# Optimization experiments

Hardware: AMD Instinct MI355X
Metric: run time of the kernel (lower is better)

The kernel has to match this reference:

```python
import jax, jax.numpy as jnp
import numpy as np


def setup_inputs() -> dict:
    key = jax.random.key(0)
    B, C, H, W = 16, 512, 56, 56
    heads, agent, win = 8, 49, 56
    ks = jax.random.split(key, 16)
    std = 0.02
    tn = lambda k, s: jax.random.truncated_normal(k, -2.0, 2.0, s, jnp.float32) * std
    return {
        "x": jax.random.normal(ks[0], (B, C, H, W), jnp.float32),
        "H": H,
        "W": W,
        "q_w": jax.random.normal(ks[1], (C, C), jnp.float32) * (C ** -0.5),
        "kv_w": jax.random.normal(ks[2], (2 * C, C), jnp.float32) * (C ** -0.5),
        "proj_w": jax.random.normal(ks[3], (C, C), jnp.float32) * (C ** -0.5),
        "proj_b": jnp.zeros((C,), jnp.float32),
        "dwc_w": jax.random.normal(ks[4], (C, 1, 3, 3), jnp.float32) * (1.0 / 3.0),
        "dwc_b": jnp.zeros((C,), jnp.float32),
        "an_bias": tn(ks[5], (heads, agent, 7, 7)),
        "na_bias": tn(ks[6], (heads, agent, 7, 7)),
        "ah_bias": tn(ks[7], (1, heads, agent, win, 1)),
        "aw_bias": tn(ks[8], (1, heads, agent, 1, win)),
        "ha_bias": tn(ks[9], (1, heads, win, 1, agent)),
        "wa_bias": tn(ks[10], (1, heads, 1, win, agent)),
    }


def reference(x, H, W, q_w, kv_w, proj_w, proj_b, dwc_w, dwc_b,
              an_bias, na_bias, ah_bias, aw_bias, ha_bias, wa_bias):
    B, C, H1, W1 = x.shape
    heads, agent = an_bias.shape[0], an_bias.shape[1]
    hd = C // heads
    scale = hd ** -0.5
    n = H1 * W1
    pool = int(agent ** 0.5)  # 7

    # NOTE: original torch code does x.view(B, H1*W1, C) on an NCHW tensor:
    # a raw row-major reshape, reproduced faithfully here.
    xf = x.reshape(B, n, C)

    q = xf @ q_w.T                       # [B, n, C]
    kv = xf @ kv_w.T                     # [B, n, 2C]
    k, v = kv[..., :C], kv[..., C:]

    # agent tokens: adaptive avg pool of q (as HxW image) to pool x pool (exact blocks)
    q_img = q.reshape(B, H, W, C)
    agent_tokens = q_img.reshape(B, pool, H // pool, pool, W // pool, C).mean(axis=(2, 4))
    agent_tokens = agent_tokens.reshape(B, agent, C)

    qh = q.reshape(B, n, heads, hd).transpose(0, 2, 1, 3)            # [B,h,n,d]
    kh = k.reshape(B, n, heads, hd).transpose(0, 2, 1, 3)            # [B,h,n,d]
    vh = v.reshape(B, n, heads, hd).transpose(0, 2, 1, 3)            # [B,h,n,d]
    ah = agent_tokens.reshape(B, agent, heads, hd).transpose(0, 2, 1, 3)  # [B,h,a,d]

    # stage 1: agent -> kv attention, with interpolated + separable position bias
    pb1 = jax.image.resize(an_bias, (heads, agent, H, W), 'bilinear').reshape(1, heads, agent, n)
    pb2 = (ah_bias + aw_bias).reshape(1, heads, agent, n)
    agent_logits = jnp.einsum('bhad,bhnd->bhan', ah * scale, kh) + pb1 + pb2
    agent_attn = jax.nn.softmax(agent_logits, axis=-1)
    agent_v = jnp.einsum('bhan,bhnd->bhad', agent_attn, vh)          # [B,h,a,d]

    # stage 2: query -> agent attention
    ab1 = jax.image.resize(na_bias, (heads, agent, H, W), 'bilinear').reshape(1, heads, agent, n)
    ab1 = ab1.transpose(0, 1, 3, 2)                                  # [1,h,n,a]
    ab2 = (ha_bias + wa_bias).reshape(1, heads, n, agent)
    q_logits = jnp.einsum('bhnd,bhad->bhna', qh * scale, ah) + ab1 + ab2
    q_attn = jax.nn.softmax(q_logits, axis=-1)
    out = jnp.einsum('bhna,bhad->bhnd', q_attn, agent_v)
    out = out.transpose(0, 2, 1, 3).reshape(B, n, C)

    # depthwise-conv residual on v (sr_ratio == 1: no interpolate)
    v_img = v.reshape(B, H, W, C).transpose(0, 3, 1, 2)              # [B,C,H,W]
    dwc = jax.lax.conv_general_dilated(
        v_img, dwc_w, window_strides=(1, 1), padding='SAME',
        feature_group_count=C, dimension_numbers=('NCHW', 'OIHW', 'NCHW'))
    dwc = dwc + dwc_b[None, :, None, None]
    out = out + dwc.transpose(0, 2, 3, 1).reshape(B, n, C)

    out = out @ proj_w.T + proj_b
    return out.reshape(B, C, H1, W1)
```

## Files before the change

### kernel.cpp

```cpp
#include <hip/hip_runtime.h>
#include <math.h>

#define B_ 16
#define C_ 512
#define Nn 3136
#define HEADS 8
#define HD 64
#define AG 49
#define Mrows (B_ * Nn)

typedef unsigned short ushortT;
typedef __attribute__((ext_vector_type(8))) short bf16x8;
typedef __attribute__((ext_vector_type(4))) float f32x4;

#define MFMA16(a, b, c) __builtin_amdgcn_mfma_f32_16x16x32_bf16((a), (b), (c), 0, 0, 0)

__device__ inline float bf2f(ushortT u) { return __uint_as_float(((unsigned)u) << 16); }
__device__ inline ushortT f2bf(float f) {
    unsigned x = __float_as_uint(f);
    unsigned r = (x + 0x7fffu + ((x >> 16) & 1u)) >> 16;
    return (ushortT)r;
}
__device__ inline f32x4 fzero4() { f32x4 z = {0.f, 0.f, 0.f, 0.f}; return z; }

__device__ inline void gl_lds16(const ushortT* g, ushortT* l) {
    __builtin_amdgcn_global_load_lds(
        (const __attribute__((address_space(1))) void*)g,
        (__attribute__((address_space(3))) void*)l, 16, 0, 0);
}

#define VMCNT(n) asm volatile("s_waitcnt vmcnt(" #n ")" ::: "memory")
#define LGKM0_SB() { asm volatile("s_waitcnt lgkmcnt(0)" ::: "memory"); \
                     __builtin_amdgcn_sched_barrier(0); }
#define BAR() __builtin_amdgcn_s_barrier()

__global__ void cvt_f2b4(const float* __restrict__ src, ushortT* __restrict__ dst, int n4) {
    int g = blockIdx.x * 256 + threadIdx.x;
    if (g >= n4) return;
    float4 v = *(const float4*)&src[(size_t)g * 4];
    ushort4 o = make_ushort4(f2bf(v.x), f2bf(v.y), f2bf(v.z), f2bf(v.w));
    *(ushort4*)&dst[(size_t)g * 4] = o;
}

__global__ void repack_w(const float* __restrict__ w, float* __restrict__ wT) {
    int g = blockIdx.x * 256 + threadIdx.x;
    if (g >= 9 * 512) return;
    int c = g % 512, tap = g / 512;
    wT[g] = w[c * 9 + tap];
}

template <int MB, int NL>
__device__ __forceinline__ void quad(f32x4 (&acc)[8][4], const bf16x8 (&af)[4][2],
                                     const bf16x8 (&bf)[4][2]) {
#pragma unroll
    for (int m = 0; m < 4; ++m)
#pragma unroll
        for (int n = 0; n < 2; ++n) {
            acc[MB + m][NL + n] = MFMA16(af[m][0], bf[NL + n][0], acc[MB + m][NL + n]);
            acc[MB + m][NL + n] = MFMA16(af[m][1], bf[NL + n][1], acc[MB + m][NL + n]);
        }
}

template <typename TO>
__global__ __launch_bounds__(512, 2)
void gemm256(const ushortT* __restrict__ A, const ushortT* __restrict__ Bw,
             const float* __restrict__ bias, TO* __restrict__ out,
             int N, int nbn) {
    __shared__ __align__(16) ushortT As[2][16384];
    __shared__ __align__(16) ushortT Bs[2][16384];
    const int t = threadIdx.x, lane = t & 63, wid = t >> 6;
    const int chunk = (int)gridDim.x >> 3;
    const int id2 = ((int)blockIdx.x & 7) * chunk + ((int)blockIdx.x >> 3);
    const int by = id2 / nbn, bx = id2 - by * nbn;
    const int m0 = by * 256, n0 = bx * 256;
    const int wm = wid >> 2, wn = wid & 3;

    const int rl0 = t >> 3;
    const int skg = (t & 7) ^ (rl0 & 7);
    const int ra0 = rl0 & 63;
    const int ra1 = (rl0 & 63) + 128;
    const int rb0 = (rl0 & 31) + ((rl0 >> 5) << 6);
    const int rb1 = rb0 + 128;
    const ushortT* gA0 = A + (size_t)(m0 + ra0) * 512 + skg * 8;
    const ushortT* gA1 = A + (size_t)(m0 + ra1) * 512 + skg * 8;
    const ushortT* gB0 = Bw + (size_t)(n0 + rb0) * 512 + skg * 8;
    const ushortT* gB1 = Bw + (size_t)(n0 + rb1) * 512 + skg * 8;
    const int bA0 = wid * 512;
    const int bA1 = wid * 512 + 8192;
    const int gbu = ((wid * 8) & 31) + (((wid * 8) >> 5) << 6);
    const int bB0 = gbu * 64;
    const int bB1 = bB0 + 8192;

#define ISSA(bufi, ro, ko) { gl_lds16(gA0 + (ro) * 512 + (ko), &As[bufi][bA0 + (ro) * 64]); \
                             gl_lds16(gA1 + (ro) * 512 + (ko), &As[bufi][bA1 + (ro) * 64]); }
#define ISSB(bufi, ro, ko) { gl_lds16(gB0 + (ro) * 512 + (ko), &Bs[bufi][bB0 + (ro) * 64]); \
                             gl_lds16(gB1 + (ro) * 512 + (ko), &Bs[bufi][bB1 + (ro) * 64]); }

    f32x4 acc[8][4];
#pragma unroll
    for (int i = 0; i < 8; ++i)
#pragma unroll
        for (int j = 0; j < 4; ++j) acc[i][j] = fzero4();

    const int r15 = lane & 15, kq16 = lane >> 4;
    const int rA = wm * 128 + r15;
    const int rB = wn * 64 + r15;
    const int sw0 = ((kq16) ^ (r15 & 7)) << 3;
    const int sw1 = ((4 + kq16) ^ (r15 & 7)) << 3;

    ISSA(0, 0, 0);
    ISSB(0, 0, 0);
    ISSB(0, 32, 0);
    ISSA(0, 64, 0);
    VMCNT(4);
    BAR();

    bf16x8 af[4][2], bf[4][2];
    for (int kt = 0; kt < 8; ++kt) {
        const ushortT* Ac = As[kt & 1];
        const ushortT* Bc = Bs[kt & 1];
        const int nb = (kt + 1) & 1;
        const int ko = (kt + 1) * 64;
        const bool pre = (kt < 7);
#pragma unroll
        for (int mt = 0; mt < 4; ++mt) {
            af[mt][0] = *(const bf16x8*)&Ac[(rA + mt * 16) * 64 + sw0];
            af[mt][1] = *(const bf16x8*)&Ac[(rA + mt * 16) * 64 + sw1];
        }
#pragma unroll
        for (int nt = 0; nt < 2; ++nt) {
            bf[nt][0] = *(const bf16x8*)&Bc[(rB + nt * 16) * 64 + sw0];
            bf[nt][1] = *(const bf16x8*)&Bc[(rB + nt * 16) * 64 + sw1];
        }
        if (pre) ISSA(nb, 0, ko);
        BAR(); LGKM0_SB();
        __builtin_amdgcn_s_setprio(1);
        quad<0, 0>(acc, af, bf);
        __builtin_amdgcn_s_setprio(0);
        if (pre) { VMCNT(4); } else { VMCNT(2); }
        BAR();
#pragma unroll
        for (int nt = 2; nt < 4; ++nt) {
            bf[nt][0] = *(const bf16x8*)&Bc[(rB + nt * 16) * 64 + sw0];
            bf[nt][1] = *(const bf16x8*)&Bc[(rB + nt * 16) * 64 + sw1];
        }
        if (pre) ISSB(nb, 0, ko);
        BAR(); LGKM0_SB();
        __builtin_amdgcn_s_setprio(1);
        quad<0, 2>(acc, af, bf);
        __builtin_amdgcn_s_setprio(0);
        if (pre) { VMCNT(4); } else { VMCNT(0); }
        BAR();
#pragma unroll
        for (int mt = 0; mt < 4; ++mt) {
            af[mt][0] = *(const bf16x8*)&Ac[(rA + 64 + mt * 16) * 64 + sw0];
            af[mt][1] = *(const bf16x8*)&Ac[(rA + 64 + mt * 16) * 64 + sw1];
        }
        if (pre) ISSB(nb, 32, ko);
        BAR(); LGKM0_SB();
        __builtin_amdgcn_s_setprio(1);
        quad<4, 0>(acc, af, bf);
        __builtin_amdgcn_s_setprio(0);
        BAR();
        if (pre) ISSA(nb, 64, ko);
        BAR(); LGKM0_SB();
        __builtin_amdgcn_s_setprio(1);
        quad<4, 2>(acc, af, bf);
        __builtin_amdgcn_s_setprio(0);
        if (pre) { VMCNT(4); }
        BAR();
    }
#undef ISSA
#undef ISSB

    const int cn = r15, rg = kq16 << 2;
#pragma unroll
    for (int mt = 0; mt < 8; ++mt) {
        int mrow = m0 + wm * 128 + mt * 16 + rg;
#pragma unroll
        for (int nt = 0; nt < 4; ++nt) {
            int ncol = n0 + wn * 64 + nt * 16 + cn;
            float bv = bias ? bias[ncol] : 0.f;
#pragma unroll
            for (int r = 0; r < 4; ++r) {
                float v = acc[mt][nt][r] + bv;
                if (sizeof(TO) == 2) ((ushortT*)out)[(size_t)(mrow + r) * N + ncol] = f2bf(v);
                else                 ((float*)out)[(size_t)(mrow + r) * N + ncol] = v;
            }
        }
    }
}

__global__ void agent_pool(const ushortT* __restrict__ qkv, float* __restrict__ at) {
    int g = blockIdx.x * 256 + threadIdx.x;
    int c8 = (g & 63) << 3;
    int a = (g >> 6) % AG;
    int b = g / (AG * 64);
    int p1 = a / 7, p2 = a % 7;
    float s[8] = {};
    for (int yy = 0; yy < 8; ++yy)
#pragma unroll
        for (int xx = 0; xx < 8; ++xx) {
            int i = (p1 * 8 + yy) * 56 + (p2 * 8 + xx);
            const ushortT* p = &qkv[(size_t)(b * Nn + i) * 1536 + c8];
            ushort4 u0 = *(const ushort4*)p;
            ushort4 u1 = *(const ushort4*)(p + 4);
            s[0] += bf2f(u0.x); s[1] += bf2f(u0.y); s[2] += bf2f(u0.z); s[3] += bf2f(u0.w);
            s[4] += bf2f(u1.x); s[5] += bf2f(u1.y); s[6] += bf2f(u1.z); s[7] += bf2f(u1.w);
        }
    float* o = &at[((size_t)(b * AG + a) << 9) + c8];
#pragma unroll
    for (int j = 0; j < 8; ++j) o[j] = s[j] * (1.f / 64.f);
}

__device__ inline float bilin7(const float* __restrict__ p, int y, int x) {
    float fy = fminf(fmaxf(y * 0.125f - 0.4375f, 0.f), 6.f);
    float fx = fminf(fmaxf(x * 0.125f - 0.4375f, 0.f), 6.f);
    int y0 = (int)fy; float ty = fy - y0; int y1 = min(y0 + 1, 6);
    int x0 = (int)fx; float tx = fx - x0; int x1 = min(x0 + 1, 6);
    float v00 = p[y0 * 7 + x0], v01 = p[y0 * 7 + x1];
    float v10 = p[y1 * 7 + x0], v11 = p[y1 * 7 + x1];
    return (1.f - ty) * ((1.f - tx) * v00 + tx * v01) + ty * ((1.f - tx) * v10 + tx * v11);
}

__global__ void bias1_k(const float* __restrict__ an, const float* __restrict__ ahb,
                        const float* __restrict__ awb, float* __restrict__ out) {
    int g = blockIdx.x * 256 + threadIdx.x;
    if (g >= HEADS * AG * Nn) return;
    int i = g % Nn; int a = (g / Nn) % AG; int h = g / (AG * Nn);
    int y = i / 56, x = i % 56;
    float v = bilin7(an + (h * AG + a) * 49, y, x);
    out[g] = v + ahb[(h * AG + a) * 56 + y] + awb[(h * AG + a) * 56 + x];
}

__global__ void bias2_k(const float* __restrict__ na, const float* __restrict__ hab,
                        const float* __restrict__ wab, float* __restrict__ out) {
    int g = blockIdx.x * 256 + threadIdx.x;
    if (g >= HEADS * Nn * AG) return;
    int a = g % AG; int i = (g / AG) % Nn; int h = g / (AG * Nn);
    int y = i / 56, x = i % 56;
    float v = bilin7(na + (h * AG + a) * 49, y, x);
    out[g] = v + hab[(h * 56 + y) * AG + a] + wab[(h * 56 + x) * AG + a];
}

__global__ void zerof(float* __restrict__ p, int nfl) {
    int g = blockIdx.x * 256 + threadIdx.x;
    if (g < nfl) p[g] = 0.f;
}

__global__ __launch_bounds__(256)
void agent_av_fused(const ushortT* __restrict__ qkv, const float* __restrict__ at,
                    const float* __restrict__ b1, float* __restrict__ num,
                    float* __restrict__ den) {
    __shared__ __align__(16) ushortT ah_s[64 * 72];
    __shared__ __align__(16) ushortT vt[64 * 72];
    __shared__ __align__(16) ushortT p_s[64 * 72];
    const int t = threadIdx.x, lane = t & 63, wid = t >> 6;
    const int bh = blockIdx.y, b = bh >> 3, h = bh & 7;
    for (int idx = t; idx < 512; idx += 256) {
        int a = idx >> 3, d8 = (idx & 7) << 3;
        bf16x8 tmp;
        if (a < AG) {
            const float* p = &at[((size_t)(b * AG + a) << 9) + (h << 6) + d8];
#pragma unroll
            for (int j = 0; j < 8; ++j) tmp[j] = (short)f2bf(p[j] * 0.125f);
        } else {
#pragma unroll
            for (int j = 0; j < 8; ++j) tmp[j] = 0;
        }
        *(bf16x8*)&ah_s[a * 72 + d8] = tmp;
    }
    __syncthreads();
    const int r15 = lane & 15, kq = (lane >> 4) << 3;
    const int rbase = (lane >> 4) << 2;
    bf16x8 af[4][2];
#pragma unroll
    for (int mt = 0; mt < 4; ++mt)
#pragma unroll
        for (int ks = 0; ks < 2; ++ks)
            af[mt][ks] = *(const bf16x8*)&ah_s[(mt * 16 + r15) * 72 + ks * 32 + kq];

    f32x4 accn[4];
#pragma unroll
    for (int nt = 0; nt < 4; ++nt) accn[nt] = fzero4();
    float denl[4][4];
#pragma unroll
    for (int mt = 0; mt < 4; ++mt)
#pragma unroll
        for (int r = 0; r < 4; ++r) denl[mt][r] = 0.f;

    const int i0b = blockIdx.x * 448;
    const int svi = t >> 2, svd = (t & 3) << 4;
    for (int cc = 0; cc < 7; ++cc) {
        const int i0 = i0b + cc * 64;
        {
            const ushortT* vp = &qkv[(size_t)(b * Nn + i0 + svi) * 1536 + 1024 + (h << 6) + svd];
            bf16x8 u0 = *(const bf16x8*)vp;
            bf16x8 u1 = *(const bf16x8*)(vp + 8);
#pragma unroll
            for (int j = 0; j < 8; ++j) {
                vt[(svd + j) * 72 + svi]     = (ushortT)u0[j];
                vt[(svd + 8 + j) * 72 + svi] = (ushortT)u1[j];
            }
        }
        {
            const int iw = i0 + wid * 16;
            const ushortT* kp = &qkv[(size_t)(b * Nn + iw + r15) * 1536 + 512 + (h << 6) + kq];
            bf16x8 bk0 = *(const bf16x8*)kp;
            bf16x8 bk1 = *(const bf16x8*)(kp + 32);
            f32x4 sacc[4];
#pragma unroll
            for (int mt = 0; mt < 4; ++mt) {
                sacc[mt] = MFMA16(af[mt][0], bk0, fzero4());
                sacc[mt] = MFMA16(af[mt][1], bk1, sacc[mt]);
            }
            const int ic = iw + r15;
#pragma unroll
            for (int mt = 0; mt < 4; ++mt)
#pragma unroll
                for (int r = 0; r < 4; ++r) {
                    int a = mt * 16 + rbase + r;
                    float e = 0.f;
                    if (a < AG)
                        e = __expf(sacc[mt][r] + b1[(size_t)(h * AG + a) * Nn + ic]);
                    denl[mt][r] += e;
                    p_s[a * 72 + wid * 16 + r15] = f2bf(e);
                }
        }
        __syncthreads();
        {
            bf16x8 ap0 = *(const bf16x8*)&p_s[(wid * 16 + r15) * 72 + kq];
            bf16x8 ap1 = *(const bf16x8*)&p_s[(wid * 16 + r15) * 72 + 32 + kq];
#pragma unroll
            for (int nt = 0; nt < 4; ++nt) {
                bf16x8 bv0 = *(const bf16x8*)&vt[(nt * 16 + r15) * 72 + kq];
                bf16x8 bv1 = *(const bf16x8*)&vt[(nt * 16 + r15) * 72 + 32 + kq];
                accn[nt] = MFMA16(ap0, bv0, accn[nt]);
                accn[nt] = MFMA16(ap1, bv1, accn[nt]);
            }
        }
        __syncthreads();
    }
#pragma unroll
    for (int r = 0; r < 4; ++r) {
        int a = wid * 16 + rbase + r;
        if (a < AG) {
#pragma unroll
            for (int nt = 0; nt < 4; ++nt)
                atomicAdd(&num[((size_t)(bh * AG + a) << 6) + nt * 16 + r15],
                          accn[nt][r]);
        }
    }
#pragma unroll
    for (int mt = 0; mt < 4; ++mt)
#pragma unroll
        for (int r = 0; r < 4; ++r) {
            float s = denl[mt][r];
#pragma unroll
            for (int off = 8; off >= 1; off >>= 1) s += __shfl_xor(s, off);
            if (r15 == 0) {
                int a = mt * 16 + rbase + r;
                if (a < AG) atomicAdd(&den[bh * AG + a], s);
            }
        }
}

__global__ __launch_bounds__(256)
void q_attn_mfma(const ushortT* __restrict__ qkv, const float* __restrict__ at,
                 const float* __restrict__ num, const float* __restrict__ den,
                 const float* __restrict__ b2, ushortT* __restrict__ attn) {
    __shared__ __align__(16) ushortT ah_s[64 * 72];
    __shared__ __align__(16) ushortT avT[64 * 72];
    __shared__ __align__(16) ushortT p_s[4][16 * 72];
    int t = threadIdx.x, lane = t & 63, wid = t >> 6;
    int bh = blockIdx.y, b = bh >> 3, h = bh & 7;
    for (int idx = t; idx < 512; idx += 256) {
        int a = idx >> 3, d8 = (idx & 7) << 3;
        bf16x8 tmp;
        if (a < AG) {
            const float* p = &at[((size_t)(b * AG + a) << 9) + (h << 6) + d8];
#pragma unroll
            for (int j = 0; j < 8; ++j) tmp[j] = (short)f2bf(p[j] * 0.125f);
        } else {
#pragma unroll
            for (int j = 0; j < 8; ++j) tmp[j] = 0;
        }
        *(bf16x8*)&ah_s[a * 72 + d8] = tmp;
    }
    for (int idx = t; idx < 4096; idx += 256) {
        int a = idx >> 6, d = idx & 63;
        float v = 0.f;
        if (a < AG)
            v = num[((size_t)(bh * AG + a) << 6) + d] / den[bh * AG + a];
        avT[d * 72 + a] = f2bf(v);
    }
    __syncthreads();
    int r15 = lane & 15, kq = (lane >> 4) << 3;
    bf16x8 bah[4][2], bav[4][2];
#pragma unroll
    for (int nt = 0; nt < 4; ++nt)
#pragma unroll
        for (int ks = 0; ks < 2; ++ks) {
            bah[nt][ks] = *(const bf16x8*)&ah_s[(nt * 16 + r15) * 72 + ks * 32 + kq];
            bav[nt][ks] = *(const bf16x8*)&avT[(nt * 16 + r15) * 72 + ks * 32 + kq];
        }
    ushortT* psw = p_s[wid];
    int i0b = blockIdx.x * 448;
    int rbase = (lane >> 4) << 2;
    for (int tt = 0; tt < 7; ++tt) {
        int i0 = i0b + (wid * 7 + tt) * 16;
        const ushortT* qp = &qkv[(size_t)(b * Nn + i0 + r15) * 1536 + (h << 6) + kq];
        bf16x8 aq0 = *(const bf16x8*)qp;
        bf16x8 aq1 = *(const bf16x8*)(qp + 32);
        f32x4 lg[4];
#pragma unroll
        for (int nt = 0; nt < 4; ++nt) {
            lg[nt] = MFMA16(aq0, bah[nt][0], fzero4());
            lg[nt] = MFMA16(aq1, bah[nt][1], lg[nt]);
        }
        float p4[4][4];
#pragma unroll
        for (int r = 0; r < 4; ++r) {
            int i = i0 + rbase + r;
            float vals[4]; float sm = 0.f;
#pragma unroll
            for (int nt = 0; nt < 4; ++nt) {
                int a = nt * 16 + r15;
                float e = 0.f;
                if (a < AG) e = __expf(lg[nt][r] + b2[(size_t)(h * Nn + i) * AG + a]);
                vals[nt] = e; sm += e;
            }
#pragma unroll
            for (int off = 8; off >= 1; off >>= 1) sm += __shfl_xor(sm, off);
            float inv = 1.f / sm;
#pragma unroll
            for (int nt = 0; nt < 4; ++nt) p4[nt][r] = vals[nt] * inv;
        }
#pragma unroll
        for (int nt = 0; nt < 4; ++nt)
#pragma unroll
            for (int r = 0; r < 4; ++r)
                psw[(rbase + r) * 72 + nt * 16 + r15] = f2bf(p4[nt][r]);
        bf16x8 ap0 = *(const bf16x8*)&psw[r15 * 72 + kq];
        bf16x8 ap1 = *(const bf16x8*)&psw[r15 * 72 + 32 + kq];
        f32x4 ov[4];
#pragma unroll
        for (int nt = 0; nt < 4; ++nt) {
            ov[nt] = MFMA16(ap0, bav[nt][0], fzero4());
            ov[nt] = MFMA16(ap1, bav[nt][1], ov[nt]);
        }
#pragma unroll
        for (int r = 0; r < 4; ++r) {
            int i = i0 + rbase + r;
            ushortT* op = &attn[(size_t)(b * Nn + i) * C_ + (h << 6)];
#pragma unroll
            for (int nt = 0; nt < 4; ++nt)
                op[nt * 16 + r15] = f2bf(ov[nt][r]);
        }
    }
}

__global__ void dwc_add_v(const ushortT* __restrict__ qkv, const float* __restrict__ wT,
                          const float* __restrict__ bb, ushortT* __restrict__ attn) {
    int g = blockIdx.x * 256 + threadIdx.x;
    int c8 = (g & 63) << 3;
    int bi = g >> 6;
    int i = bi % Nn;
    int y = i / 56, x = i % 56;
    float acc[8];
    {
        float4 b0 = *(const float4*)&bb[c8];
        float4 b1 = *(const float4*)&bb[c8 + 4];
        acc[0] = b0.x; acc[1] = b0.y; acc[2] = b0.z; acc[3] = b0.w;
        acc[4] = b1.x; acc[5] = b1.y; acc[6] = b1.z; acc[7] = b1.w;
    }
#pragma unroll
    for (int dy = -1; dy <= 1; ++dy) {
        int yy = y + dy; if (yy < 0 || yy > 55) continue;
#pragma unroll
        for (int dx = -1; dx <= 1; ++dx) {
            int xx = x + dx; if (xx < 0 || xx > 55) continue;
            const ushortT* vp = &qkv[(size_t)(bi + dy * 56 + dx) * 1536 + 1024 + c8];
            ushort4 u0 = *(const ushort4*)vp;
            ushort4 u1 = *(const ushort4*)(vp + 4);
            const float* wp = &wT[((dy + 1) * 3 + dx + 1) * 512 + c8];
            float4 w0 = *(const float4*)wp;
            float4 w1 = *(const float4*)(wp + 4);
            acc[0] += bf2f(u0.x) * w0.x; acc[1] += bf2f(u0.y) * w0.y;
            acc[2] += bf2f(u0.z) * w0.z; acc[3] += bf2f(u0.w) * w0.w;
            acc[4] += bf2f(u1.x) * w1.x; acc[5] += bf2f(u1.y) * w1.y;
            acc[6] += bf2f(u1.z) * w1.z; acc[7] += bf2f(u1.w) * w1.w;
        }
    }
    ushortT* op = &attn[(size_t)bi * C_ + c8];
    ushort4 a0 = *(const ushort4*)op;
    ushort4 a1 = *(const ushort4*)(op + 4);
    ushort4 o0 = make_ushort4(f2bf(bf2f(a0.x) + acc[0]), f2bf(bf2f(a0.y) + acc[1]),
                              f2bf(bf2f(a0.z) + acc[2]), f2bf(bf2f(a0.w) + acc[3]));
    ushort4 o1 = make_ushort4(f2bf(bf2f(a1.x) + acc[4]), f2bf(bf2f(a1.y) + acc[5]),
                              f2bf(bf2f(a1.z) + acc[6]), f2bf(bf2f(a1.w) + acc[7]));
    *(ushort4*)op = o0; *(ushort4*)(op + 4) = o1;
}

extern "C" void kernel_launch(void* const* d_in, const int* in_sizes, int n_in,
                              void* d_out, int out_size, void* d_ws, size_t ws_size,
                              hipStream_t stream) {
    const float* x      = (const float*)d_in[0];
    const float* q_w    = (const float*)d_in[3];
    const float* kv_w   = (const float*)d_in[4];
    const float* proj_w = (const float*)d_in[5];
    const float* proj_b = (const float*)d_in[6];
    const float* dwc_w  = (const float*)d_in[7];
    const float* dwc_b  = (const float*)d_in[8];
    const float* an_b   = (const float*)d_in[9];
    const float* na_b   = (const float*)d_in[10];
    const float* ah_b   = (const float*)d_in[11];
    const float* aw_b   = (const float*)d_in[12];
    const float* ha_b   = (const float*)d_in[13];
    const float* wa_b   = (const float*)d_in[14];
    float* out = (float*)d_out;

    char* ws = (char*)d_ws;
    ushortT* R    = (ushortT*)(ws);
    ushortT* qkv  = (ushortT*)(ws + 51380224);
    ushortT* Wqkv = (ushortT*)(ws + 205520896);
    ushortT* Wp   = (ushortT*)(ws + 207093760);
    float*   wT   = (float*)(ws + 207618048);
    float*   at   = (float*)(ws + 207636480);
    float*   b1   = (float*)(ws + 209242112);
    float*   b2   = (float*)(ws + 214159360);
    float*   num  = (float*)(ws + 219076608);
    float*   den  = (float*)Wqkv;
    ushortT* xb   = R;
    ushortT* attn = R;

    cvt_f2b4<<<25088, 256, 0, stream>>>(x, xb, 6422528);
    cvt_f2b4<<<256,   256, 0, stream>>>(q_w, Wqkv, 65536);
    cvt_f2b4<<<512,   256, 0, stream>>>(kv_w, Wqkv + 262144, 131072);
    cvt_f2b4<<<256,   256, 0, stream>>>(proj_w, Wp, 65536);
    repack_w<<<18,    256, 0, stream>>>(dwc_w, wT);
    gemm256<ushortT><<<1176, 512, 0, stream>>>(xb, Wqkv, nullptr, qkv, 1536, 6);
    agent_pool<<<196, 256, 0, stream>>>(qkv, at);
    bias1_k<<<4802, 256, 0, stream>>>(an_b, ah_b, aw_b, b1);
    bias2_k<<<4802, 256, 0, stream>>>(na_b, ha_b, wa_b, b2);
    zerof<<<1568, 256, 0, stream>>>(num, B_ * HEADS * AG * HD);
    zerof<<<25,   256, 0, stream>>>(den, B_ * HEADS * AG);
    agent_av_fused<<<dim3(7, 128), 256, 0, stream>>>(qkv, at, b1, num, den);
    q_attn_mfma<<<dim3(7, 128), 256, 0, stream>>>(qkv, at, num, den, b2, attn);
    dwc_add_v<<<12544, 256, 0, stream>>>(qkv, wT, dwc_b, attn);
    gemm256<float><<<392, 512, 0, stream>>>(attn, Wp, proj_b, out, 512, 2);
}
```

Before: 536.9 us.

## Merge small kernels, parallelize agent pooling, and simplify GEMM prefetch schedule

Weight conversions, the two bias-map kernels and the two zero-fill kernels are each folded into a single launch to cut launch overhead. The agent pooling kernel now gives each (batch, agent) pair its own block, splitting the 64 pooled positions across four thread groups and combining them with a shared-memory reduction, so far more blocks run in parallel. The QKV/proj GEMM main loop issues the whole next tile's A and B loads early and waits once per iteration instead of interleaving waits. This may expose more memory latency or reduce overlap at the single wait point.

```diff
diff --git a/kernel.cpp b/kernel.cpp
--- a/kernel.cpp
+++ b/kernel.cpp
@@ -42,11 +42,24 @@
     *(ushort4*)&dst[(size_t)g * 4] = o;
 }
 
-__global__ void repack_w(const float* __restrict__ w, float* __restrict__ wT) {
+__global__ void cvt_weights(const float* __restrict__ qw, const float* __restrict__ kvw,
+                            const float* __restrict__ pw, const float* __restrict__ dwcw,
+                            ushortT* __restrict__ Wqkv, ushortT* __restrict__ Wp,
+                            float* __restrict__ wT) {
     int g = blockIdx.x * 256 + threadIdx.x;
-    if (g >= 9 * 512) return;
-    int c = g % 512, tap = g / 512;
-    wT[g] = w[c * 9 + tap];
+    if (g < 196608) {
+        const float* src = (g < 65536) ? &qw[(size_t)g * 4] : &kvw[(size_t)(g - 65536) * 4];
+        float4 v = *(const float4*)src;
+        *(ushort4*)&Wqkv[(size_t)g * 4] =
+            make_ushort4(f2bf(v.x), f2bf(v.y), f2bf(v.z), f2bf(v.w));
+    } else if (g < 262144) {
+        float4 v = *(const float4*)&pw[(size_t)(g - 196608) * 4];
+        *(ushort4*)&Wp[(size_t)(g - 196608) * 4] =
+            make_ushort4(f2bf(v.x), f2bf(v.y), f2bf(v.z), f2bf(v.w));
+    } else {
+        int gg = g - 262144;
+        if (gg < 4608) { int c = gg & 511, tap = gg >> 9; wT[gg] = dwcw[c * 9 + tap]; }
+    }
 }
 
 template <int MB, int NL>
@@ -108,11 +121,9 @@
     const int sw0 = ((kq16) ^ (r15 & 7)) << 3;
     const int sw1 = ((4 + kq16) ^ (r15 & 7)) << 3;
 
-    ISSA(0, 0, 0);
-    ISSB(0, 0, 0);
-    ISSB(0, 32, 0);
-    ISSA(0, 64, 0);
-    VMCNT(4);
+    ISSA(0, 0, 0); ISSA(0, 64, 0);
+    ISSB(0, 0, 0); ISSB(0, 32, 0);
+    VMCNT(0);
     BAR();
 
     bf16x8 af[4][2], bf[4][2];
@@ -132,42 +143,37 @@
             bf[nt][0] = *(const bf16x8*)&Bc[(rB + nt * 16) * 64 + sw0];
             bf[nt][1] = *(const bf16x8*)&Bc[(rB + nt * 16) * 64 + sw1];
         }
-        if (pre) ISSA(nb, 0, ko);
+        if (pre) { ISSA(nb, 0, ko); ISSA(nb, 64, ko); }
         BAR(); LGKM0_SB();
         __builtin_amdgcn_s_setprio(1);
         quad<0, 0>(acc, af, bf);
         __builtin_amdgcn_s_setprio(0);
-        if (pre) { VMCNT(4); } else { VMCNT(2); }
         BAR();
 #pragma unroll
         for (int nt = 2; nt < 4; ++nt) {
             bf[nt][0] = *(const bf16x8*)&Bc[(rB + nt * 16) * 64 + sw0];
             bf[nt][1] = *(const bf16x8*)&Bc[(rB + nt * 16) * 64 + sw1];
         }
-        if (pre) ISSB(nb, 0, ko);
+        if (pre) { ISSB(nb, 0, ko); ISSB(nb, 32, ko); }
         BAR(); LGKM0_SB();
         __builtin_amdgcn_s_setprio(1);
         quad<0, 2>(acc, af, bf);
         __builtin_amdgcn_s_setprio(0);
-        if (pre) { VMCNT(4); } else { VMCNT(0); }
         BAR();
 #pragma unroll
         for (int mt = 0; mt < 4; ++mt) {
             af[mt][0] = *(const bf16x8*)&Ac[(rA + 64 + mt * 16) * 64 + sw0];
             af[mt][1] = *(const bf16x8*)&Ac[(rA + 64 + mt * 16) * 64 + sw1];
         }
-        if (pre) ISSB(nb, 32, ko);
         BAR(); LGKM0_SB();
         __builtin_amdgcn_s_setprio(1);
         quad<4, 0>(acc, af, bf);
         __builtin_amdgcn_s_setprio(0);
         BAR();
-        if (pre) ISSA(nb, 64, ko);
-        BAR(); LGKM0_SB();
         __builtin_amdgcn_s_setprio(1);
         quad<4, 2>(acc, af, bf);
         __builtin_amdgcn_s_setprio(0);
-        if (pre) { VMCNT(4); }
+        if (pre) { VMCNT(0); }
         BAR();
     }
 #undef ISSA
@@ -191,26 +197,33 @@
     }
 }
 
-__global__ void agent_pool(const ushortT* __restrict__ qkv, float* __restrict__ at) {
-    int g = blockIdx.x * 256 + threadIdx.x;
-    int c8 = (g & 63) << 3;
-    int a = (g >> 6) % AG;
-    int b = g / (AG * 64);
+__global__ __launch_bounds__(256)
+void agent_pool(const ushortT* __restrict__ qkv, float* __restrict__ at) {
+    __shared__ float red[256][9];
+    int t = threadIdx.x;
+    int ba = blockIdx.x;
+    int b = ba / AG, a = ba % AG;
+    int c8 = (t & 63) << 3, qr = t >> 6;
     int p1 = a / 7, p2 = a % 7;
     float s[8] = {};
-    for (int yy = 0; yy < 8; ++yy)
-#pragma unroll
-        for (int xx = 0; xx < 8; ++xx) {
-            int i = (p1 * 8 + yy) * 56 + (p2 * 8 + xx);
-            const ushortT* p = &qkv[(size_t)(b * Nn + i) * 1536 + c8];
-            ushort4 u0 = *(const ushort4*)p;
-            ushort4 u1 = *(const ushort4*)(p + 4);
-            s[0] += bf2f(u0.x); s[1] += bf2f(u0.y); s[2] += bf2f(u0.z); s[3] += bf2f(u0.w);
-            s[4] += bf2f(u1.x); s[5] += bf2f(u1.y); s[6] += bf2f(u1.z); s[7] += bf2f(u1.w);
-        }
-    float* o = &at[((size_t)(b * AG + a) << 9) + c8];
-#pragma unroll
-    for (int j = 0; j < 8; ++j) o[j] = s[j] * (1.f / 64.f);
+#pragma unroll
+    for (int pp = 0; pp < 16; ++pp) {
+        int pos = (qr << 4) + pp;
+        int i = (p1 * 8 + (pos >> 3)) * 56 + p2 * 8 + (pos & 7);
+        bf16x8 u = *(const bf16x8*)&qkv[(size_t)(b * Nn + i) * 1536 + c8];
+#pragma unroll
+        for (int j = 0; j < 8; ++j) s[j] += bf2f((ushortT)u[j]);
+    }
+#pragma unroll
+    for (int j = 0; j < 8; ++j) red[t][j] = s[j];
+    __syncthreads();
+    if (t < 64) {
+        float* o = &at[((size_t)(b * AG + a) << 9) + (t << 3)];
+#pragma unroll
+        for (int j = 0; j < 8; ++j)
+            o[j] = (red[t][j] + red[t + 64][j] + red[t + 128][j] + red[t + 192][j])
+                   * (1.f / 64.f);
+    }
 }
 
 __device__ inline float bilin7(const float* __restrict__ p, int y, int x) {
@@ -223,29 +236,30 @@
     return (1.f - ty) * ((1.f - tx) * v00 + tx * v01) + ty * ((1.f - tx) * v10 + tx * v11);
 }
 
-__global__ void bias1_k(const float* __restrict__ an, const float* __restrict__ ahb,
-                        const float* __restrict__ awb, float* __restrict__ out) {
+__global__ void bias_k(const float* __restrict__ an, const float* __restrict__ ahb,
+                       const float* __restrict__ awb, const float* __restrict__ na,
+                       const float* __restrict__ hab, const float* __restrict__ wab,
+                       float* __restrict__ b1, float* __restrict__ b2) {
     int g = blockIdx.x * 256 + threadIdx.x;
-    if (g >= HEADS * AG * Nn) return;
-    int i = g % Nn; int a = (g / Nn) % AG; int h = g / (AG * Nn);
-    int y = i / 56, x = i % 56;
-    float v = bilin7(an + (h * AG + a) * 49, y, x);
-    out[g] = v + ahb[(h * AG + a) * 56 + y] + awb[(h * AG + a) * 56 + x];
-}
-
-__global__ void bias2_k(const float* __restrict__ na, const float* __restrict__ hab,
-                        const float* __restrict__ wab, float* __restrict__ out) {
+    const int NT = HEADS * AG * Nn;
+    if (g < NT) {
+        int i = g % Nn; int a = (g / Nn) % AG; int h = g / (AG * Nn);
+        int y = i / 56, x = i % 56;
+        b1[g] = bilin7(an + (h * AG + a) * 49, y, x)
+              + ahb[(h * AG + a) * 56 + y] + awb[(h * AG + a) * 56 + x];
+    } else {
+        g -= NT; if (g >= NT) return;
+        int a = g % AG; int i = (g / AG) % Nn; int h = g / (AG * Nn);
+        int y = i / 56, x = i % 56;
+        b2[g] = bilin7(na + (h * AG + a) * 49, y, x)
+              + hab[(h * 56 + y) * AG + a] + wab[(h * 56 + x) * AG + a];
+    }
+}
+
+__global__ void zero2(float* __restrict__ num, int n1, float* __restrict__ den, int n2) {
     int g = blockIdx.x * 256 + threadIdx.x;
-    if (g >= HEADS * Nn * AG) return;
-    int a = g % AG; int i = (g / AG) % Nn; int h = g / (AG * Nn);
-    int y = i / 56, x = i % 56;
-    float v = bilin7(na + (h * AG + a) * 49, y, x);
-    out[g] = v + hab[(h * 56 + y) * AG + a] + wab[(h * 56 + x) * AG + a];
-}
-
-__global__ void zerof(float* __restrict__ p, int nfl) {
-    int g = blockIdx.x * 256 + threadIdx.x;
-    if (g < nfl) p[g] = 0.f;
+    if (g < n1) num[g] = 0.f;
+    else if (g - n1 < n2) den[g - n1] = 0.f;
 }
 
 __global__ __launch_bounds__(256)
@@ -535,16 +549,11 @@
     ushortT* attn = R;
 
     cvt_f2b4<<<25088, 256, 0, stream>>>(x, xb, 6422528);
-    cvt_f2b4<<<256,   256, 0, stream>>>(q_w, Wqkv, 65536);
-    cvt_f2b4<<<512,   256, 0, stream>>>(kv_w, Wqkv + 262144, 131072);
-    cvt_f2b4<<<256,   256, 0, stream>>>(proj_w, Wp, 65536);
-    repack_w<<<18,    256, 0, stream>>>(dwc_w, wT);
+    cvt_weights<<<1042, 256, 0, stream>>>(q_w, kv_w, proj_w, dwc_w, Wqkv, Wp, wT);
     gemm256<ushortT><<<1176, 512, 0, stream>>>(xb, Wqkv, nullptr, qkv, 1536, 6);
-    agent_pool<<<196, 256, 0, stream>>>(qkv, at);
-    bias1_k<<<4802, 256, 0, stream>>>(an_b, ah_b, aw_b, b1);
-    bias2_k<<<4802, 256, 0, stream>>>(na_b, ha_b, wa_b, b2);
-    zerof<<<1568, 256, 0, stream>>>(num, B_ * HEADS * AG * HD);
-    zerof<<<25,   256, 0, stream>>>(den, B_ * HEADS * AG);
+    agent_pool<<<784, 256, 0, stream>>>(qkv, at);
+    bias_k<<<9604, 256, 0, stream>>>(an_b, ah_b, aw_b, na_b, ha_b, wa_b, b1, b2);
+    zero2<<<1593, 256, 0, stream>>>(num, B_ * HEADS * AG * HD, den, B_ * HEADS * AG);
     agent_av_fused<<<dim3(7, 128), 256, 0, stream>>>(qkv, at, b1, num, den);
     q_attn_mfma<<<dim3(7, 128), 256, 0, stream>>>(qkv, at, num, den, b2, attn);
     dwc_add_v<<<12544, 256, 0, stream>>>(qkv, wT, dwc_b, attn);
```

New measurement: 527.5 us. Within noise of the previous version (-1.8%).
